# Optimization experiments

Measured on AMD Instinct MI355X. Metric: run time of the kernel, lower is better.

The kernel has to match this reference:

```python
import jax, jax.numpy as jnp
import numpy as np


def setup_inputs() -> dict:
    key = jax.random.key(0)
    kq, kk, kv, km = jax.random.split(key, 4)
    B, H, S, D = 4, 16, 1024, 64
    return {
        "Q": jax.random.normal(kq, (B, H, S, D), dtype=jnp.float32),
        "K": jax.random.normal(kk, (B, H, S, D), dtype=jnp.float32),
        "V": jax.random.normal(kv, (B, H, S, D), dtype=jnp.float32),
        "attn_mask": jax.random.uniform(km, (B, H, S, S), dtype=jnp.float32),
        "d_k": 64,
    }


def reference(Q, K, V, attn_mask, d_k):
    # scores = Q K^T / sqrt(d_k): [B,H,S,S]
    scale = 1.0 / np.sqrt(d_k).astype(np.float32)
    scores = jnp.einsum("bhsd,bhtd->bhst", Q, K) * scale
    # NOTE: mask applied via matmul with mask^T (not additive) — faithful to source
    scores = jnp.einsum("bhst,bhut->bhsu", scores, attn_mask)
    attn = jax.nn.softmax(scores, axis=-1)
    context = jnp.einsum("bhst,bhtd->bhsd", attn, V)
    return (context, attn)
```

## Files before the change

kernel.cpp:

```cpp
#include <hip/hip_runtime.h>
#include <hip/hip_bf16.h>


#define BH   64
#define S    1024
#define D    64
#define SCALE 0.125f

static __device__ __forceinline__ void fma4(float4& a, float s, const float4& b) {
    a.x = fmaf(s, b.x, a.x);
    a.y = fmaf(s, b.y, a.y);
    a.z = fmaf(s, b.z, a.z);
    a.w = fmaf(s, b.w, a.w);
}

template <bool TRANS_OUT>
__global__ __launch_bounds__(256) void gemm_ab(const float* __restrict__ A,
                                               const float* __restrict__ B,
                                               float* __restrict__ C) {
    const int bh  = blockIdx.y;
    const int u0  = blockIdx.x * 64;
    const int tid = threadIdx.x;
    const int tx  = tid & 15;
    const int ty  = tid >> 4;

    __shared__ float As[64][68];
    __shared__ float Bs[64][64];

    const float* Ab = A + (size_t)bh * S * S;
    const float* Bb = B + (size_t)bh * S * D;

    float4 acc[4];
#pragma unroll
    for (int i = 0; i < 4; i++) acc[i] = make_float4(0.f, 0.f, 0.f, 0.f);

    const int lr = tid >> 4;
    const int lc = (tid & 15) * 4;

    for (int t0 = 0; t0 < S; t0 += 64) {
#pragma unroll
        for (int k = 0; k < 4; k++) {
            float4 va = *(const float4*)&Ab[(size_t)(u0 + lr + 16 * k) * S + t0 + lc];
            *(float4*)&As[lr + 16 * k][lc] = va;
            float4 vb = *(const float4*)&Bb[(size_t)(t0 + lr + 16 * k) * D + lc];
            *(float4*)&Bs[lr + 16 * k][lc] = vb;
        }
        __syncthreads();
#pragma unroll
        for (int tt = 0; tt < 64; tt += 4) {
            float4 b0 = *(const float4*)&Bs[tt + 0][tx * 4];
            float4 b1 = *(const float4*)&Bs[tt + 1][tx * 4];
            float4 b2 = *(const float4*)&Bs[tt + 2][tx * 4];
            float4 b3 = *(const float4*)&Bs[tt + 3][tx * 4];
#pragma unroll
            for (int i = 0; i < 4; i++) {
                float4 a = *(const float4*)&As[ty * 4 + i][tt];
                fma4(acc[i], a.x, b0);
                fma4(acc[i], a.y, b1);
                fma4(acc[i], a.z, b2);
                fma4(acc[i], a.w, b3);
            }
        }
        __syncthreads();
    }

    if (TRANS_OUT) {
        float* Cb = C + (size_t)bh * D * S;
#pragma unroll
        for (int i = 0; i < 4; i++) {
            const int u = u0 + ty * 4 + i;
            Cb[(size_t)(tx * 4 + 0) * S + u] = acc[i].x;
            Cb[(size_t)(tx * 4 + 1) * S + u] = acc[i].y;
            Cb[(size_t)(tx * 4 + 2) * S + u] = acc[i].z;
            Cb[(size_t)(tx * 4 + 3) * S + u] = acc[i].w;
        }
    } else {
        float* Cb = C + (size_t)bh * S * D;
#pragma unroll
        for (int i = 0; i < 4; i++) {
            *(float4*)&Cb[(size_t)(u0 + ty * 4 + i) * D + tx * 4] = acc[i];
        }
    }
}

__global__ __launch_bounds__(256) void logits_softmax(const float* __restrict__ Q,
                                                      const float* __restrict__ M2T,
                                                      float* __restrict__ attn) {
    const int bh  = blockIdx.y;
    const int s0  = blockIdx.x * 16;
    const int tid = threadIdx.x;
    const int w   = tid >> 6;
    const int l   = tid & 63;

    __shared__ float Qs[16][68];
    {
        const int r = tid >> 4;
        const int c = (tid & 15) * 4;
        float4 v = *(const float4*)&Q[((size_t)bh * S + s0 + r) * D + c];
        v.x *= SCALE; v.y *= SCALE; v.z *= SCALE; v.w *= SCALE;
        *(float4*)&Qs[r][c] = v;
    }
    __syncthreads();

    float4 acc[4][4];
#pragma unroll
    for (int r = 0; r < 4; r++)
#pragma unroll
        for (int c = 0; c < 4; c++) acc[r][c] = make_float4(0.f, 0.f, 0.f, 0.f);

    const float* M2b = M2T + (size_t)bh * D * S;

#pragma unroll 4
    for (int d = 0; d < D; d++) {
        const float* row = M2b + (size_t)d * S;
        float4 m0 = *(const float4*)&row[0 * 256 + 4 * l];
        float4 m1 = *(const float4*)&row[1 * 256 + 4 * l];
        float4 m2 = *(const float4*)&row[2 * 256 + 4 * l];
        float4 m3 = *(const float4*)&row[3 * 256 + 4 * l];
        float q0 = Qs[w * 4 + 0][d];
        float q1 = Qs[w * 4 + 1][d];
        float q2 = Qs[w * 4 + 2][d];
        float q3 = Qs[w * 4 + 3][d];
        fma4(acc[0][0], q0, m0); fma4(acc[0][1], q0, m1); fma4(acc[0][2], q0, m2); fma4(acc[0][3], q0, m3);
        fma4(acc[1][0], q1, m0); fma4(acc[1][1], q1, m1); fma4(acc[1][2], q1, m2); fma4(acc[1][3], q1, m3);
        fma4(acc[2][0], q2, m0); fma4(acc[2][1], q2, m1); fma4(acc[2][2], q2, m2); fma4(acc[2][3], q2, m3);
        fma4(acc[3][0], q3, m0); fma4(acc[3][1], q3, m1); fma4(acc[3][2], q3, m2); fma4(acc[3][3], q3, m3);
    }

#pragma unroll
    for (int r = 0; r < 4; r++) {
        const int s = s0 + w * 4 + r;
        float mx = -3.0e38f;
#pragma unroll
        for (int c = 0; c < 4; c++) {
            float4 v = acc[r][c];
            mx = fmaxf(mx, fmaxf(fmaxf(v.x, v.y), fmaxf(v.z, v.w)));
        }
#pragma unroll
        for (int off = 32; off >= 1; off >>= 1) mx = fmaxf(mx, __shfl_xor(mx, off));
        float sum = 0.f;
#pragma unroll
        for (int c = 0; c < 4; c++) {
            float4 v = acc[r][c];
            v.x = __expf(v.x - mx); v.y = __expf(v.y - mx);
            v.z = __expf(v.z - mx); v.w = __expf(v.w - mx);
            acc[r][c] = v;
            sum += v.x + v.y + v.z + v.w;
        }
#pragma unroll
        for (int off = 32; off >= 1; off >>= 1) sum += __shfl_xor(sum, off);
        const float inv = 1.0f / sum;
        float* out = attn + ((size_t)bh * S + s) * S;
#pragma unroll
        for (int c = 0; c < 4; c++) {
            float4 v = acc[r][c];
            v.x *= inv; v.y *= inv; v.z *= inv; v.w *= inv;
            *(float4*)&out[c * 256 + 4 * l] = v;
        }
    }
}

extern "C" void kernel_launch(void* const* d_in, const int* in_sizes, int n_in,
                              void* d_out, int out_size, void* d_ws, size_t ws_size,
                              hipStream_t stream) {
    const float* Q    = (const float*)d_in[0];
    const float* K    = (const float*)d_in[1];
    const float* V    = (const float*)d_in[2];
    const float* mask = (const float*)d_in[3];
    float* context = (float*)d_out;
    float* attn    = (float*)d_out + (size_t)BH * S * D;
    float* M2T     = (float*)d_ws;

    gemm_ab<true><<<dim3(16, BH), 256, 0, stream>>>(mask, K, M2T);
    logits_softmax<<<dim3(64, BH), 256, 0, stream>>>(Q, M2T, attn);
    gemm_ab<false><<<dim3(16, BH), 256, 0, stream>>>(attn, V, context);
}
```

Before: 780.5 us.

## Use split-bf16 MFMA for mask·K and attn·V GEMMs with pre-transposed operands

Replaces the scalar FP32 FMA GEMMs with MFMA 16x16x32 bf16 instructions. Operands are split into high and low bf16 parts, and three products are summed to approximate FP32 accuracy. K and V are transposed and split once in a new pre-pass kernel. The A tiles are split on the fly into swizzled LDS. This adds a kernel launch, extra workspace traffic and conversion ALU work, and carries some loss of precision from dropping the low×low term.

```diff
diff --git a/kernel.cpp b/kernel.cpp
--- a/kernel.cpp
+++ b/kernel.cpp
@@ -1,11 +1,21 @@
 #include <hip/hip_runtime.h>
-#include <hip/hip_bf16.h>
 
 
 #define BH   64
 #define S    1024
 #define D    64
 #define SCALE 0.125f
+
+typedef __attribute__((ext_vector_type(8))) short  short8;
+typedef __attribute__((ext_vector_type(4))) float  f32x4;
+
+static __device__ __forceinline__ unsigned short f2bf(float x) {
+    unsigned int u = __float_as_uint(x);
+    return (unsigned short)((u + 0x7fffu + ((u >> 16) & 1u)) >> 16);
+}
+static __device__ __forceinline__ float bf2f(unsigned short h) {
+    return __uint_as_float(((unsigned int)h) << 16);
+}
 
 static __device__ __forceinline__ void fma4(float4& a, float s, const float4& b) {
     a.x = fmaf(s, b.x, a.x);
@@ -14,72 +24,182 @@
     a.w = fmaf(s, b.w, a.w);
 }
 
+__global__ __launch_bounds__(256) void transpose_split(
+        const float* __restrict__ K, const float* __restrict__ V,
+        unsigned short* __restrict__ Kth, unsigned short* __restrict__ Ktl,
+        unsigned short* __restrict__ Vth, unsigned short* __restrict__ Vtl) {
+    const int bh = blockIdx.y;
+    const int t0 = blockIdx.x * 64;
+    const float* src      = (blockIdx.z == 0) ? K   : V;
+    unsigned short* dsth  = (blockIdx.z == 0) ? Kth : Vth;
+    unsigned short* dstl  = (blockIdx.z == 0) ? Ktl : Vtl;
+    const int tid = threadIdx.x;
+
+    __shared__ float T[64][68];
+    {
+        const int r = tid >> 4;
+        const int c = (tid & 15) * 4;
+#pragma unroll
+        for (int i = 0; i < 4; i++) {
+            float4 v = *(const float4*)&src[((size_t)bh * S + t0 + r + 16 * i) * D + c];
+            *(float4*)&T[r + 16 * i][c] = v;
+        }
+    }
+    __syncthreads();
+
+    const int d = tid >> 2;
+    const int u = (tid & 3) * 16;
+    unsigned int hw[8], lw[8];
+#pragma unroll
+    for (int j = 0; j < 8; j++) {
+        float x0 = T[u + 2 * j + 0][d];
+        float x1 = T[u + 2 * j + 1][d];
+        unsigned short h0 = f2bf(x0), h1 = f2bf(x1);
+        unsigned short l0 = f2bf(x0 - bf2f(h0)), l1 = f2bf(x1 - bf2f(h1));
+        hw[j] = (unsigned)h0 | ((unsigned)h1 << 16);
+        lw[j] = (unsigned)l0 | ((unsigned)l1 << 16);
+    }
+    const size_t o = ((size_t)bh * D + d) * S + t0 + u;
+    uint4 hv0 = {hw[0], hw[1], hw[2], hw[3]};
+    uint4 hv1 = {hw[4], hw[5], hw[6], hw[7]};
+    uint4 lv0 = {lw[0], lw[1], lw[2], lw[3]};
+    uint4 lv1 = {lw[4], lw[5], lw[6], lw[7]};
+    *(uint4*)&dsth[o]     = hv0;
+    *(uint4*)&dsth[o + 8] = hv1;
+    *(uint4*)&dstl[o]     = lv0;
+    *(uint4*)&dstl[o + 8] = lv1;
+}
+
 template <bool TRANS_OUT>
-__global__ __launch_bounds__(256) void gemm_ab(const float* __restrict__ A,
-                                               const float* __restrict__ B,
-                                               float* __restrict__ C) {
+__global__ __launch_bounds__(256) void gemm_mfma(
+        const float* __restrict__ A,
+        const unsigned short* __restrict__ Bth,
+        const unsigned short* __restrict__ Btl,
+        float* __restrict__ C) {
     const int bh  = blockIdx.y;
     const int u0  = blockIdx.x * 64;
     const int tid = threadIdx.x;
-    const int tx  = tid & 15;
-    const int ty  = tid >> 4;
-
-    __shared__ float As[64][68];
-    __shared__ float Bs[64][64];
-
-    const float* Ab = A + (size_t)bh * S * S;
-    const float* Bb = B + (size_t)bh * S * D;
-
-    float4 acc[4];
-#pragma unroll
-    for (int i = 0; i < 4; i++) acc[i] = make_float4(0.f, 0.f, 0.f, 0.f);
-
-    const int lr = tid >> 4;
-    const int lc = (tid & 15) * 4;
+
+    __shared__ __align__(16) char lds[4 * 8192];
+    char* Ah = lds;
+    char* Al = lds + 8192;
+    char* Bh = lds + 16384;
+    char* Bl = lds + 24576;
+
+    const float*          Ab  = A   + (size_t)bh * S * S + (size_t)u0 * S;
+    const unsigned short* Bhb = Bth + (size_t)bh * D * S;
+    const unsigned short* Blb = Btl + (size_t)bh * D * S;
+
+    const int wid = tid >> 6;
+    const int l   = tid & 63;
+    const int wm  = wid >> 1, wn = wid & 1;
+    const int lr  = l & 15,   lg = l >> 4;
+
+    f32x4 zero = {0.f, 0.f, 0.f, 0.f};
+    f32x4 acc[2][2];
+    acc[0][0] = zero; acc[0][1] = zero; acc[1][0] = zero; acc[1][1] = zero;
+
+    const int ar = tid >> 4;
+    const int ac = (tid & 15) * 4;
+    const int br = tid >> 2;
+    const int bc = (tid & 3) * 16;
 
     for (int t0 = 0; t0 < S; t0 += 64) {
 #pragma unroll
-        for (int k = 0; k < 4; k++) {
-            float4 va = *(const float4*)&Ab[(size_t)(u0 + lr + 16 * k) * S + t0 + lc];
-            *(float4*)&As[lr + 16 * k][lc] = va;
-            float4 vb = *(const float4*)&Bb[(size_t)(t0 + lr + 16 * k) * D + lc];
-            *(float4*)&Bs[lr + 16 * k][lc] = vb;
+        for (int i = 0; i < 4; i++) {
+            const int row = ar + 16 * i;
+            float4 v = *(const float4*)&Ab[(size_t)row * S + t0 + ac];
+            ushort4 h4, l4;
+            h4.x = f2bf(v.x); l4.x = f2bf(v.x - bf2f(h4.x));
+            h4.y = f2bf(v.y); l4.y = f2bf(v.y - bf2f(h4.y));
+            h4.z = f2bf(v.z); l4.z = f2bf(v.z - bf2f(h4.z));
+            h4.w = f2bf(v.w); l4.w = f2bf(v.w - bf2f(h4.w));
+            const int off = (row * 128 + ac * 2) ^ ((row & 7) << 4);
+            *(ushort4*)(Ah + off) = h4;
+            *(ushort4*)(Al + off) = l4;
+        }
+        {
+            const size_t g   = (size_t)br * S + t0 + bc;
+            const int base   = br * 128 + bc * 2;
+            const int sw     = (br & 7) << 4;
+            *(uint4*)(Bh + ((base     ) ^ sw)) = *(const uint4*)&Bhb[g];
+            *(uint4*)(Bh + ((base + 16) ^ sw)) = *(const uint4*)&Bhb[g + 8];
+            *(uint4*)(Bl + ((base     ) ^ sw)) = *(const uint4*)&Blb[g];
+            *(uint4*)(Bl + ((base + 16) ^ sw)) = *(const uint4*)&Blb[g + 8];
         }
         __syncthreads();
-#pragma unroll
-        for (int tt = 0; tt < 64; tt += 4) {
-            float4 b0 = *(const float4*)&Bs[tt + 0][tx * 4];
-            float4 b1 = *(const float4*)&Bs[tt + 1][tx * 4];
-            float4 b2 = *(const float4*)&Bs[tt + 2][tx * 4];
-            float4 b3 = *(const float4*)&Bs[tt + 3][tx * 4];
-#pragma unroll
-            for (int i = 0; i < 4; i++) {
-                float4 a = *(const float4*)&As[ty * 4 + i][tt];
-                fma4(acc[i], a.x, b0);
-                fma4(acc[i], a.y, b1);
-                fma4(acc[i], a.z, b2);
-                fma4(acc[i], a.w, b3);
+
+#pragma unroll
+        for (int kk = 0; kk < 2; kk++) {
+            short8 a_h[2], a_l[2], b_h[2], b_l[2];
+#pragma unroll
+            for (int mi = 0; mi < 2; mi++) {
+                const int row = wm * 32 + mi * 16 + lr;
+                const int off = (row * 128 + kk * 64 + lg * 16) ^ ((row & 7) << 4);
+                a_h[mi] = *(const short8*)(Ah + off);
+                a_l[mi] = *(const short8*)(Al + off);
             }
+#pragma unroll
+            for (int nj = 0; nj < 2; nj++) {
+                const int col = wn * 32 + nj * 16 + lr;
+                const int off = (col * 128 + kk * 64 + lg * 16) ^ ((col & 7) << 4);
+                b_h[nj] = *(const short8*)(Bh + off);
+                b_l[nj] = *(const short8*)(Bl + off);
+            }
+#pragma unroll
+            for (int mi = 0; mi < 2; mi++)
+#pragma unroll
+                for (int nj = 0; nj < 2; nj++) {
+                    acc[mi][nj] = __builtin_amdgcn_mfma_f32_16x16x32_bf16(
+                        a_h[mi], b_h[nj], acc[mi][nj], 0, 0, 0);
+                    acc[mi][nj] = __builtin_amdgcn_mfma_f32_16x16x32_bf16(
+                        a_h[mi], b_l[nj], acc[mi][nj], 0, 0, 0);
+                    acc[mi][nj] = __builtin_amdgcn_mfma_f32_16x16x32_bf16(
+                        a_l[mi], b_h[nj], acc[mi][nj], 0, 0, 0);
+                }
         }
         __syncthreads();
     }
 
     if (TRANS_OUT) {
+        float (*Cs)[68] = (float(*)[68])lds;
+#pragma unroll
+        for (int mi = 0; mi < 2; mi++)
+#pragma unroll
+            for (int nj = 0; nj < 2; nj++) {
+                const int col = wn * 32 + nj * 16 + lr;
+#pragma unroll
+                for (int r = 0; r < 4; r++) {
+                    const int row = wm * 32 + mi * 16 + lg * 4 + r;
+                    Cs[row][col] = acc[mi][nj][r];
+                }
+            }
+        __syncthreads();
         float* Cb = C + (size_t)bh * D * S;
-#pragma unroll
-        for (int i = 0; i < 4; i++) {
-            const int u = u0 + ty * 4 + i;
-            Cb[(size_t)(tx * 4 + 0) * S + u] = acc[i].x;
-            Cb[(size_t)(tx * 4 + 1) * S + u] = acc[i].y;
-            Cb[(size_t)(tx * 4 + 2) * S + u] = acc[i].z;
-            Cb[(size_t)(tx * 4 + 3) * S + u] = acc[i].w;
+        const int d  = tid >> 2;
+        const int ub = (tid & 3) * 16;
+#pragma unroll
+        for (int g = 0; g < 4; g++) {
+            float4 v;
+            v.x = Cs[ub + 4 * g + 0][d];
+            v.y = Cs[ub + 4 * g + 1][d];
+            v.z = Cs[ub + 4 * g + 2][d];
+            v.w = Cs[ub + 4 * g + 3][d];
+            *(float4*)&Cb[(size_t)d * S + u0 + ub + 4 * g] = v;
         }
     } else {
         float* Cb = C + (size_t)bh * S * D;
 #pragma unroll
-        for (int i = 0; i < 4; i++) {
-            *(float4*)&Cb[(size_t)(u0 + ty * 4 + i) * D + tx * 4] = acc[i];
-        }
+        for (int mi = 0; mi < 2; mi++)
+#pragma unroll
+            for (int nj = 0; nj < 2; nj++) {
+                const int col = wn * 32 + nj * 16 + lr;
+#pragma unroll
+                for (int r = 0; r < 4; r++) {
+                    const int row = u0 + wm * 32 + mi * 16 + lg * 4 + r;
+                    Cb[(size_t)row * D + col] = acc[mi][nj][r];
+                }
+            }
     }
 }
 
@@ -169,9 +289,15 @@
     const float* mask = (const float*)d_in[3];
     float* context = (float*)d_out;
     float* attn    = (float*)d_out + (size_t)BH * S * D;
-    float* M2T     = (float*)d_ws;
-
-    gemm_ab<true><<<dim3(16, BH), 256, 0, stream>>>(mask, K, M2T);
+
+    float* M2T = (float*)d_ws;
+    unsigned short* Kth = (unsigned short*)((char*)d_ws + (size_t)BH * D * S * sizeof(float));
+    unsigned short* Ktl = Kth + (size_t)BH * D * S;
+    unsigned short* Vth = Ktl + (size_t)BH * D * S;
+    unsigned short* Vtl = Vth + (size_t)BH * D * S;
+
+    transpose_split<<<dim3(16, BH, 2), 256, 0, stream>>>(K, V, Kth, Ktl, Vth, Vtl);
+    gemm_mfma<true><<<dim3(16, BH), 256, 0, stream>>>(mask, Kth, Ktl, M2T);
     logits_softmax<<<dim3(64, BH), 256, 0, stream>>>(Q, M2T, attn);
-    gemm_ab<false><<<dim3(16, BH), 256, 0, stream>>>(attn, V, context);
-}
+    gemm_mfma<false><<<dim3(16, BH), 256, 0, stream>>>(attn, Vth, Vtl, context);
+}
```

New measurement: 697.7 us. -10.6%, faster.
